# Performance work log

Measured on AMD Instinct MI355X. Metric: run time of the kernel, lower is better.

The kernel has to match this reference:

```python
import jax, jax.numpy as jnp
import numpy as np

B, N, IN_DIM, OUT_DIM, H = 8, 1024, 512, 512, 8
SUP = OUT_DIM // H  # support_dim per head = 64


def setup_inputs() -> dict:
    key = jax.random.key(0)
    ks = jax.random.split(key, 6)
    # 0/1 dense adjacency with self-loops so no row is fully masked
    A = jax.random.randint(ks[0], (B, N, N), 0, 2).astype(jnp.float32)
    A = jnp.maximum(A, jnp.eye(N, dtype=jnp.float32)[None])
    X = jax.random.normal(ks[1], (B, N, IN_DIM), dtype=jnp.float32)
    # parameters, uniform(-1/sqrt(fan_last), 1/sqrt(fan_last)) as in reset_parameters
    sw = 1.0 / np.sqrt(SUP)
    W = jax.random.uniform(ks[2], (H, IN_DIM, SUP), minval=-sw, maxval=sw, dtype=jnp.float32)
    w1 = jax.random.uniform(ks[3], (H, SUP), minval=-sw, maxval=sw, dtype=jnp.float32)
    w2 = jax.random.uniform(ks[4], (H, SUP), minval=-sw, maxval=sw, dtype=jnp.float32)
    b = jax.random.uniform(ks[5], (2, H), minval=-1.0, maxval=1.0, dtype=jnp.float32)
    b1, b2 = b[0], b[1]
    return {"A": A, "X": X, "W": W, "w1": w1, "b1": b1, "w2": w2, "b2": b2}


def reference(A, X, W, w1, b1, w2, b2):
    # per-head projection: [B,H,N,SUP]
    inputs = jnp.einsum('bni,hio->bhno', X, W)
    # additive attention logits: self_fc [B,H,N,1] + neigh_fc [B,H,1,N]
    self_fc = jnp.einsum('bhno,ho->bhn', inputs, w1) + b1[None, :, None]
    neigh_fc = jnp.einsum('bhno,ho->bhn', inputs, w2) + b2[None, :, None]
    logits = jax.nn.leaky_relu(self_fc[..., :, None] + neigh_fc[..., None, :], 0.01)
    mask = -1e9 * (1.0 - A)  # [B,N,N]
    alphas = jax.nn.softmax(logits + mask[:, None], axis=-1)  # [B,H,N,N]
    out = jnp.einsum('bhnm,bhmo->bhno', alphas, inputs)
    out = jax.nn.relu(out)  # default activation = torch.relu
    # concat heads on last dim (head i contiguous), matching torch.cat
    return out.transpose(0, 2, 1, 3).reshape(B, N, H * SUP)
```

## Files before the change

### kernel.cpp

```cpp
#include <hip/hip_runtime.h>
#include <hip/hip_fp16.h>

#define BB 8
#define NN 1024
#define IN_DIM 512
#define HH 8
#define SUP 64
#define HS (HH * SUP)

typedef _Float16 half8 __attribute__((ext_vector_type(8)));
typedef _Float16 half4v __attribute__((ext_vector_type(4)));
typedef _Float16 half2v __attribute__((ext_vector_type(2)));
typedef float floatx4 __attribute__((ext_vector_type(4)));

__global__ __launch_bounds__(256) void kprep(const float* __restrict__ A,
                                             unsigned char* __restrict__ Am,
                                             const float* __restrict__ W,
                                             _Float16* __restrict__ Wt,
                                             const float* __restrict__ X,
                                             _Float16* __restrict__ Xh) {
    __shared__ float tile[64][65];
    const int bid = blockIdx.x;
    const int t   = threadIdx.x;
    if (bid < 2048) {
        const int gw   = bid * 4 + (t >> 6);
        const int lane = t & 63;
        const float* arow = A + (size_t)gw * NN;
        unsigned long long keep = 0;
#pragma unroll
        for (int g = 0; g < 16; g++) {
            float a = arow[g * 64 + lane];
            unsigned long long bal = __ballot(a > 0.5f);
            if (lane == g) keep = bal;
        }
        if (lane < 16)
            *(unsigned long long*)(Am + (size_t)gw * 128 + lane * 8) = keep;
    } else if (bid < 2112) {
        const int wb = bid - 2048;
        const int it = wb & 7;
        const int h  = wb >> 3;
        {
            const int i  = t >> 2;
            const int o0 = (t & 3) * 16;
            const float* src = W + ((size_t)h * IN_DIM + it * 64 + i) * SUP + o0;
#pragma unroll
            for (int j = 0; j < 4; j++) {
                float4 v = ((const float4*)src)[j];
                tile[i][o0 + j * 4 + 0] = v.x;
                tile[i][o0 + j * 4 + 1] = v.y;
                tile[i][o0 + j * 4 + 2] = v.z;
                tile[i][o0 + j * 4 + 3] = v.w;
            }
        }
        __syncthreads();
        {
            const int o  = t >> 2;
            const int i0 = (t & 3) * 16;
            _Float16 buf[16];
#pragma unroll
            for (int j = 0; j < 16; j++) buf[j] = (_Float16)tile[i0 + j][o];
            _Float16* dst = Wt + ((size_t)h * SUP + o) * IN_DIM + it * 64 + i0;
            *(half8*)dst       = *(half8*)buf;
            *(half8*)(dst + 8) = *(half8*)(buf + 8);
        }
    } else {
        const int xb = bid - 2112;
#pragma unroll 4
        for (int i = 0; i < 32; i++) {
            const size_t idx = (((size_t)xb * 32 + i) * 256 + t) * 4;
            float4 v = *(const float4*)(X + idx);
            half4v h = {(_Float16)v.x, (_Float16)v.y, (_Float16)v.z, (_Float16)v.w};
            *(half4v*)(Xh + idx) = h;
        }
    }
}

__global__ __launch_bounds__(256) void k1_proj(const _Float16* __restrict__ Xh,
                                               const _Float16* __restrict__ Wt,
                                               const float* __restrict__ w1,
                                               const float* __restrict__ b1,
                                               const float* __restrict__ w2,
                                               const float* __restrict__ b2,
                                               _Float16* __restrict__ Pt,
                                               float* __restrict__ s_g,
                                               float* __restrict__ t_g,
                                               float* __restrict__ tmax16) {
    __shared__ __align__(16) _Float16 po[64 * 72];
    __shared__ float tred[64];

    const int bh = blockIdx.y;
    const int b  = bh >> 3;
    const int h  = bh & 7;
    const int n0 = blockIdx.x * 64;
    const int t    = threadIdx.x;
    const int wave = t >> 6;
    const int lane = t & 63;
    const int quad = lane >> 4;
    const int l15  = lane & 15;

    floatx4 acc[4];
#pragma unroll
    for (int i = 0; i < 4; i++) acc[i] = {0.f, 0.f, 0.f, 0.f};

    float w1v[4], w2v[4];
#pragma unroll
    for (int ct = 0; ct < 4; ct++) {
        w1v[ct] = w1[h * 64 + ct * 16 + l15];
        w2v[ct] = w2[h * 64 + ct * 16 + l15];
    }
    const float b1h = b1[h];
    const float b2h = b2[h];

    const _Float16* xf = Xh + ((size_t)(b * NN + n0 + wave * 16 + l15)) * IN_DIM + quad * 8;
    const _Float16* wf = Wt + ((size_t)(h * SUP + l15)) * IN_DIM + quad * 8;

#pragma unroll 4
    for (int k0 = 0; k0 < IN_DIM; k0 += 32) {
        half8 af  = *(const half8*)(xf + k0);
        half8 bf0 = *(const half8*)(wf + k0);
        half8 bf1 = *(const half8*)(wf + 16 * IN_DIM + k0);
        half8 bf2 = *(const half8*)(wf + 32 * IN_DIM + k0);
        half8 bf3 = *(const half8*)(wf + 48 * IN_DIM + k0);
        acc[0] = __builtin_amdgcn_mfma_f32_16x16x32_f16(af, bf0, acc[0], 0, 0, 0);
        acc[1] = __builtin_amdgcn_mfma_f32_16x16x32_f16(af, bf1, acc[1], 0, 0, 0);
        acc[2] = __builtin_amdgcn_mfma_f32_16x16x32_f16(af, bf2, acc[2], 0, 0, 0);
        acc[3] = __builtin_amdgcn_mfma_f32_16x16x32_f16(af, bf3, acc[3], 0, 0, 0);
    }

#pragma unroll
    for (int ct = 0; ct < 4; ct++) {
#pragma unroll
        for (int r = 0; r < 4; r++) {
            int o = ct * 16 + l15;
            int n = wave * 16 + quad * 4 + r;
            po[o * 72 + n] = (_Float16)acc[ct][r];
        }
    }
#pragma unroll
    for (int r = 0; r < 4; r++) {
        float sp = 0.f, tp = 0.f;
#pragma unroll
        for (int ct = 0; ct < 4; ct++) {
            sp += acc[ct][r] * w1v[ct];
            tp += acc[ct][r] * w2v[ct];
        }
#pragma unroll
        for (int off = 1; off < 16; off <<= 1) {
            sp += __shfl_xor(sp, off);
            tp += __shfl_xor(tp, off);
        }
        if (l15 == 0) {
            const int n = wave * 16 + quad * 4 + r;
            s_g[(size_t)bh * NN + n0 + n] = sp + b1h;
            float tv = tp + b2h;
            t_g[(size_t)bh * NN + n0 + n] = tv;
            tred[n] = tv;
        }
    }
    __syncthreads();
    {
        const int o   = t >> 2;
        const int nof = (t & 3) * 16;
        _Float16* dst = Pt + ((size_t)bh * SUP + o) * NN + n0 + nof;
        *(half8*)dst       = *(const half8*)&po[o * 72 + nof];
        *(half8*)(dst + 8) = *(const half8*)&po[o * 72 + nof + 8];
    }
    if (t == 0) {
        float m = -1e30f;
#pragma unroll
        for (int i = 0; i < 64; i++) m = fmaxf(m, tred[i]);
        tmax16[bh * 16 + blockIdx.x] = m;
    }
}

__global__ __launch_bounds__(512) void k2_attn(const unsigned char* __restrict__ Am,
                                               const _Float16* __restrict__ Pt,
                                               const float* __restrict__ s_g,
                                               const float* __restrict__ t_g,
                                               const float* __restrict__ tmax16,
                                               float* __restrict__ out) {
    __shared__ __align__(16) _Float16 vts[2][64 * 136];
    __shared__ __align__(16) unsigned t2l[NN / 2];
    __shared__ __align__(16) uint4 lutm[256];

    const int bh = blockIdx.y;
    const int b  = bh >> 3;
    const int h  = bh & 7;
    const int n0 = blockIdx.x * 128;
    const int t    = threadIdx.x;
    const int wave = t >> 6;
    const int lane = t & 63;
    const int quad = lane >> 4;
    const int l15  = lane & 15;
    const int row4 = t >> 3;
    const int seg  = t & 7;

    {
        float2 tv2 = ((const float2*)(t_g + (size_t)bh * NN))[t];
        half2v tp = {(_Float16)tv2.x, (_Float16)tv2.y};
        t2l[t] = *(unsigned*)&tp;
    }
    if (t < 256) {
        unsigned e = (unsigned)t;
        uint4 v;
        v.x = ((e & 1u)   ? 0xFFFFu : 0u) | ((e & 2u)   ? 0xFFFF0000u : 0u);
        v.y = ((e & 4u)   ? 0xFFFFu : 0u) | ((e & 8u)   ? 0xFFFF0000u : 0u);
        v.z = ((e & 16u)  ? 0xFFFFu : 0u) | ((e & 32u)  ? 0xFFFF0000u : 0u);
        v.w = ((e & 64u)  ? 0xFFFFu : 0u) | ((e & 128u) ? 0xFFFF0000u : 0u);
        lutm[t] = v;
    }

    float tmax = -1e30f;
#pragma unroll
    for (int i = 0; i < 16; i++) tmax = fmaxf(tmax, tmax16[bh * 16 + i]);

    const int myrow = wave * 16 + l15;
    const float sv = s_g[(size_t)bh * NN + n0 + myrow];
    const float xc = sv + tmax;
    const float cv = fmaxf(xc, 0.01f * xc);
    const float l2e = 1.44269504f;
    const _Float16 sc1h = (_Float16)((sv - cv) * l2e);
    const _Float16 sc2h = (_Float16)(-0.99f * cv * l2e);
    const half2v sc1 = {sc1h, sc1h};
    const half2v sc2 = {sc2h, sc2h};
    const half2v vl2e = {(_Float16)l2e, (_Float16)l2e};
    const half2v v001 = {(_Float16)0.01f, (_Float16)0.01f};
    const half2v ones2 = {(_Float16)1.0f, (_Float16)1.0f};

    floatx4 acc[4];
#pragma unroll
    for (int i = 0; i < 4; i++) acc[i] = {0.f, 0.f, 0.f, 0.f};
    float zp = 0.f;

    const _Float16* pb = Pt + ((size_t)bh * SUP + row4) * NN + seg * 16;
    half8 v0 = ((const half8*)pb)[0];
    half8 v1 = ((const half8*)pb)[1];
    const uint4* mrow = (const uint4*)(Am + ((size_t)b * NN + n0 + myrow) * 128);
    uint4 mcur = mrow[0];

    for (int mt = 0; mt < 8; mt++) {
        const int cur = mt & 1;
        {
            _Float16* d = &vts[cur][row4 * 136 + seg * 16];
            ((half8*)d)[0] = v0;
            ((half8*)d)[1] = v1;
        }
        __syncthreads();
        uint4 mnext;
        if (mt < 7) {
            const _Float16* p = pb + (mt + 1) * 128;
            v0 = ((const half8*)p)[0];
            v1 = ((const half8*)p)[1];
            mnext = mrow[mt + 1];
        }
        const unsigned mw[4] = {mcur.x, mcur.y, mcur.z, mcur.w};
#pragma unroll
        for (int kk = 0; kk < 4; kk++) {
            const unsigned mbyte = (mw[kk] >> (quad * 8)) & 0xffu;
            uint4 mx = lutm[mbyte];
            const unsigned mxw[4] = {mx.x, mx.y, mx.z, mx.w};
            uint4 tw = *(const uint4*)&t2l[mt * 64 + kk * 16 + quad * 4];
            union { uint4 u; half2v h[4]; } tt; tt.u = tw;
            union { half2v h[4]; half8 h8; } wbu;
#pragma unroll
            for (int p = 0; p < 4; p++) {
                half2v y = tt.h[p] * vl2e + sc1;
                half2v w = y * v001 + sc2;
                half2v z = __builtin_elementwise_max(y, w);
                __half2 zz = *(__half2*)&z;
                __half2 ee = h2exp2(zz);
                unsigned eb = (*(unsigned*)&ee) & mxw[p];
                half2v e2 = *(half2v*)&eb;
#if __has_builtin(__builtin_amdgcn_fdot2)
                zp = __builtin_amdgcn_fdot2(e2, ones2, zp, false);
#else
                zp += (float)e2.x + (float)e2.y;
#endif
                wbu.h[p] = e2;
            }
            half8 af = wbu.h8;
#pragma unroll
            for (int ct = 0; ct < 4; ct++) {
                half8 bf = *(const half8*)&vts[cur][(ct * 16 + l15) * 136 + kk * 32 + quad * 8];
                acc[ct] = __builtin_amdgcn_mfma_f32_16x16x32_f16(af, bf, acc[ct], 0, 0, 0);
            }
        }
        if (mt < 7) mcur = mnext;
    }

    zp += __shfl_xor(zp, 16);
    zp += __shfl_xor(zp, 32);
    const float rzown = 1.0f / zp;

#pragma unroll
    for (int r = 0; r < 4; r++) {
        const int rr = wave * 16 + quad * 4 + r;
        const float rz = __shfl(rzown, quad * 20 + r);
#pragma unroll
        for (int ct = 0; ct < 4; ct++) {
            float v = acc[ct][r] * rz;
            v = v > 0.f ? v : 0.f;
            out[((size_t)b * NN + n0 + rr) * HS + h * SUP + ct * 16 + l15] = v;
        }
    }
}

extern "C" void kernel_launch(void* const* d_in, const int* in_sizes, int n_in,
                              void* d_out, int out_size, void* d_ws, size_t ws_size,
                              hipStream_t stream) {
    const float* A  = (const float*)d_in[0];
    const float* X  = (const float*)d_in[1];
    const float* W  = (const float*)d_in[2];
    const float* w1 = (const float*)d_in[3];
    const float* b1 = (const float*)d_in[4];
    const float* w2 = (const float*)d_in[5];
    const float* b2 = (const float*)d_in[6];
    float* out = (float*)d_out;

    char* ws = (char*)d_ws;
    _Float16*      Wt     = (_Float16*)(ws);
    _Float16*      Pt     = (_Float16*)(ws + 524288);
    float*         s_g    = (float*)(ws + 8912896);
    float*         t_g    = (float*)(ws + 9175040);
    float*         tmax16 = (float*)(ws + 9437184);
    unsigned char* Am     = (unsigned char*)(ws + 9441280);
    _Float16*      Xh     = (_Float16*)(ws + 10489856);

    hipLaunchKernelGGL(kprep, dim3(2048 + 64 + 128), dim3(256), 0, stream, A, Am, W, Wt, X, Xh);
    hipLaunchKernelGGL(k1_proj, dim3(NN / 64, BB * HH), dim3(256), 0, stream,
                       Xh, Wt, w1, b1, w2, b2, Pt, s_g, t_g, tmax16);
    hipLaunchKernelGGL(k2_attn, dim3(NN / 128, BB * HH), dim3(512), 0, stream,
                       Am, Pt, s_g, t_g, tmax16, out);
}
```

Before: 159.6 us.

## Stage X and W tiles through double-buffered LDS in projection GEMM

The projection kernel now loads 64x32 tiles of X and W cooperatively into double-buffered shared memory, with each thread fetching one 16-byte chunk, and prefetches the next tile into registers while computing on the current one. Previously every wave loaded all four W fragments straight from global memory, so W was read redundantly by the four waves. The change cuts redundant global traffic and makes loads coalesced. In exchange it adds a __syncthreads per k-step and extra LDS use.

```diff
diff --git a/kernel.cpp b/kernel.cpp
--- a/kernel.cpp
+++ b/kernel.cpp
@@ -85,6 +85,8 @@
                                                float* __restrict__ s_g,
                                                float* __restrict__ t_g,
                                                float* __restrict__ tmax16) {
+    __shared__ __align__(16) _Float16 xs[2][64 * 40];
+    __shared__ __align__(16) _Float16 wsh[2][64 * 40];
     __shared__ __align__(16) _Float16 po[64 * 72];
     __shared__ float tred[64];
 
@@ -97,6 +99,8 @@
     const int lane = t & 63;
     const int quad = lane >> 4;
     const int l15  = lane & 15;
+    const int row  = t >> 2;
+    const int koff = (t & 3) * 8;
 
     floatx4 acc[4];
 #pragma unroll
@@ -111,21 +115,29 @@
     const float b1h = b1[h];
     const float b2h = b2[h];
 
-    const _Float16* xf = Xh + ((size_t)(b * NN + n0 + wave * 16 + l15)) * IN_DIM + quad * 8;
-    const _Float16* wf = Wt + ((size_t)(h * SUP + l15)) * IN_DIM + quad * 8;
-
-#pragma unroll 4
-    for (int k0 = 0; k0 < IN_DIM; k0 += 32) {
-        half8 af  = *(const half8*)(xf + k0);
-        half8 bf0 = *(const half8*)(wf + k0);
-        half8 bf1 = *(const half8*)(wf + 16 * IN_DIM + k0);
-        half8 bf2 = *(const half8*)(wf + 32 * IN_DIM + k0);
-        half8 bf3 = *(const half8*)(wf + 48 * IN_DIM + k0);
-        acc[0] = __builtin_amdgcn_mfma_f32_16x16x32_f16(af, bf0, acc[0], 0, 0, 0);
-        acc[1] = __builtin_amdgcn_mfma_f32_16x16x32_f16(af, bf1, acc[1], 0, 0, 0);
-        acc[2] = __builtin_amdgcn_mfma_f32_16x16x32_f16(af, bf2, acc[2], 0, 0, 0);
-        acc[3] = __builtin_amdgcn_mfma_f32_16x16x32_f16(af, bf3, acc[3], 0, 0, 0);
-    }
+    const _Float16* xbase = Xh + ((size_t)b * NN + n0 + row) * IN_DIM + koff;
+    const _Float16* wbase = Wt + ((size_t)h * SUP + row) * IN_DIM + koff;
+
+    half8 xv = *(const half8*)xbase;
+    half8 wv = *(const half8*)wbase;
+
+    for (int it = 0; it < 16; it++) {
+        const int cur = it & 1;
+        *(half8*)&xs[cur][row * 40 + koff]  = xv;
+        *(half8*)&wsh[cur][row * 40 + koff] = wv;
+        __syncthreads();
+        if (it < 15) {
+            xv = *(const half8*)(xbase + (it + 1) * 32);
+            wv = *(const half8*)(wbase + (it + 1) * 32);
+        }
+        half8 af = *(const half8*)&xs[cur][(wave * 16 + l15) * 40 + quad * 8];
+#pragma unroll
+        for (int ct = 0; ct < 4; ct++) {
+            half8 bf = *(const half8*)&wsh[cur][(ct * 16 + l15) * 40 + quad * 8];
+            acc[ct] = __builtin_amdgcn_mfma_f32_16x16x32_f16(af, bf, acc[ct], 0, 0, 0);
+        }
+    }
+    __syncthreads();
 
 #pragma unroll
     for (int ct = 0; ct < 4; ct++) {
```

New measurement: 137.2 us. -14.0%, faster.
